# Performance work log

Hardware: AMD Instinct MI355X
Metric: run time of the kernel (lower is better)

The kernel has to match this reference:

```python
import jax, jax.numpy as jnp
import numpy as np

DIM = 256
HEADS = 8
DIM_HEAD = 32
HIDDEN = HEADS * DIM_HEAD  # 256
SCALE = DIM_HEAD ** -0.5


def setup_inputs() -> dict:
    key = jax.random.key(0)
    k1, k2, k3, k4 = jax.random.split(key, 4)
    x = jax.random.normal(k1, (1, DIM, 16, 16, 16), dtype=jnp.float32)
    # 1x1x1 Conv3d weights are plain channel-mixing matrices
    w_qkv = jax.random.normal(k2, (3 * HIDDEN, DIM), dtype=jnp.float32) * (DIM ** -0.5)
    w_out = jax.random.normal(k3, (DIM, HIDDEN), dtype=jnp.float32) * (HIDDEN ** -0.5)
    b_out = jax.random.normal(k4, (DIM,), dtype=jnp.float32) * 0.01
    return {"x": x, "w_qkv": w_qkv, "w_out": w_out, "b_out": b_out}


def reference(x, w_qkv, w_out, b_out):
    b, c, X, Y, Z = x.shape
    n = X * Y * Z
    xf = x.reshape(b, c, n)                                   # b c n
    qkv = jnp.einsum('oc,bcn->bon', w_qkv, xf)                # b 3H n
    q, k, v = jnp.split(qkv, 3, axis=1)                       # each b (h c) n
    def heads(t):
        return t.reshape(b, HEADS, DIM_HEAD, n)               # b h c n
    q, k, v = heads(q) * SCALE, heads(k), heads(v)
    sim = jnp.einsum('bhci,bhcj->bhij', q, k)                 # b h n n
    attn = jax.nn.softmax(sim, axis=-1)
    out = jnp.einsum('bhij,bhcj->bhci', attn, v)              # b h c n
    out = out.reshape(b, HIDDEN, n)                           # b (h c) n
    out = jnp.einsum('oc,bcn->bon', w_out, out) + b_out[None, :, None]
    return out.reshape(b, DIM, X, Y, Z)
```

## Files before the change

kernel.cpp:

```cpp
#include <hip/hip_runtime.h>
#include <hip/hip_bf16.h>
#include <cstdint>


typedef __bf16 bf16x8 __attribute__((ext_vector_type(8)));
typedef float f32x4 __attribute__((ext_vector_type(4)));
typedef float f32x16 __attribute__((ext_vector_type(16)));
typedef unsigned int u32;
typedef unsigned short u16;
typedef u32 u32x4v __attribute__((ext_vector_type(4)));
typedef u32 u32x2v __attribute__((ext_vector_type(2)));

#define MFMA16(a, b, c) __builtin_amdgcn_mfma_f32_16x16x32_bf16(a, b, c, 0, 0, 0)
#define MFMA32(a, b, c) __builtin_amdgcn_mfma_f32_32x32x16_bf16(a, b, c, 0, 0, 0)

#if __has_builtin(__builtin_amdgcn_exp2f)
#define EXP2(x) __builtin_amdgcn_exp2f(x)
#else
#define EXP2(x) exp2f(x)
#endif

__device__ __forceinline__ u16 f2bf(float f) {
  __bf16 b = (__bf16)f;
  return __builtin_bit_cast(u16, b);
}
__device__ __forceinline__ u32 pk2(float a, float b) {
  return (u32)f2bf(a) | ((u32)f2bf(b) << 16);
}
__device__ __forceinline__ bf16x8 ldfrag(const u16* p) {
  return __builtin_bit_cast(bf16x8, *(const u32x4v*)p);
}
__device__ __forceinline__ void gload_lds16(const void* g, void* l) {
  __builtin_amdgcn_global_load_lds((const __attribute__((address_space(1))) u32*)g,
                                   (__attribute__((address_space(3))) u32*)l, 16, 0, 0);
}
__device__ __forceinline__ void plswap(u32& a, u32& b) {
  asm("v_permlane32_swap_b32 %0, %1" : "+v"(a), "+v"(b));
}
__device__ __forceinline__ f32x16 zero16() {
  f32x16 z;
#pragma unroll
  for (int i = 0; i < 16; ++i) z[i] = 0.0f;
  return z;
}

#if __has_builtin(__builtin_amdgcn_fdot2_f32_bf16)
typedef __bf16 bf16x2 __attribute__((ext_vector_type(2)));
__device__ __forceinline__ float dot2one(u32 pk, float acc) {
  const u32 one2 = 0x3F803F80u;
  return __builtin_amdgcn_fdot2_f32_bf16(__builtin_bit_cast(bf16x2, pk),
                                         __builtin_bit_cast(bf16x2, one2), acc, false);
}
#define LSUM4(LSUM, PK0, PK1, PK2, PK3) \
  LSUM = dot2one(PK0, LSUM);            \
  LSUM = dot2one(PK1, LSUM);            \
  LSUM = dot2one(PK2, LSUM);            \
  LSUM = dot2one(PK3, LSUM);
#define LSUM_F32(LSUM, ...)
#else
#define LSUM4(LSUM, PK0, PK1, PK2, PK3)
#define LSUM_F32(LSUM, P0, P1, P2, P3, P4, P5, P6, P7) \
  LSUM += ((P0 + P1) + (P2 + P3)) + ((P4 + P5) + (P6 + P7));
#endif

__global__ __launch_bounds__(256) void prep(const float* __restrict__ x,
                                            const float* __restrict__ wq,
                                            const float* __restrict__ wo,
                                            u16* __restrict__ xT, u16* __restrict__ wqb,
                                            u16* __restrict__ wob) {
  const int b = blockIdx.x;
  const int t = threadIdx.x;
  if (b < 256) {
    __shared__ u16 tile[64][72];
    const int n0 = (b & 63) * 64, c0 = (b >> 6) * 64;
#pragma unroll
    for (int r = 0; r < 4; ++r) {
      int c = r * 16 + (t >> 4);
      int n4 = (t & 15) << 2;
      float4 v = *(const float4*)(x + (size_t)(c0 + c) * 4096 + n0 + n4);
      tile[n4 + 0][c] = f2bf(v.x);
      tile[n4 + 1][c] = f2bf(v.y);
      tile[n4 + 2][c] = f2bf(v.z);
      tile[n4 + 3][c] = f2bf(v.w);
    }
    __syncthreads();
#pragma unroll
    for (int r2 = 0; r2 < 2; ++r2) {
      int n = r2 * 32 + (t >> 3);
      int c8 = (t & 7) << 3;
      u32x4v o;
#pragma unroll
      for (int j = 0; j < 4; ++j)
        o[j] = (u32)tile[n][c8 + 2 * j] | ((u32)tile[n][c8 + 2 * j + 1] << 16);
      *(u32x4v*)(xT + (size_t)(n0 + n) * 256 + c0 + c8) = o;
    }
  } else if (b < 304) {
    int base = (b - 256) * 4096;
#pragma unroll
    for (int r = 0; r < 4; ++r) {
      int i = base + r * 1024 + t * 4;
      float4 v = *(const float4*)(wq + i);
      float sc = (i < 65536) ? 0.2550349f : 1.0f;
      u32x2v pkd;
      pkd.x = pk2(v.x * sc, v.y * sc);
      pkd.y = pk2(v.z * sc, v.w * sc);
      *(u32x2v*)(wqb + i) = pkd;
    }
  } else {
    int base = (b - 304) * 4096;
#pragma unroll
    for (int r = 0; r < 4; ++r) {
      int i = base + r * 1024 + t * 4;
      float4 v = *(const float4*)(wo + i);
      u32x2v pkd;
      pkd.x = pk2(v.x, v.y);
      pkd.y = pk2(v.z, v.w);
      *(u32x2v*)(wob + i) = pkd;
    }
  }
}

__global__ __launch_bounds__(256) void qkv_gemm(const u16* __restrict__ xT,
                                                const u16* __restrict__ wqb,
                                                u16* __restrict__ qT, u16* __restrict__ kT,
                                                u16* __restrict__ vv) {
  __shared__ __align__(16) u16 Al[64 * 64];
  __shared__ __align__(16) u16 Bl[64 * 64];
  const int t = threadIdx.x;
  const int lane = t & 63, w = t >> 6;
  const int wm = w & 1, wn = w >> 1;
  const int o0 = blockIdx.y * 64, n0 = blockIdx.x * 64;
  const int lr = lane & 15, lg = lane >> 4;
  const int srow = lane >> 3, sslot = lane & 7;
  f32x4 acc[2][2];
#pragma unroll
  for (int i = 0; i < 2; ++i)
#pragma unroll
    for (int j = 0; j < 2; ++j)
#pragma unroll
      for (int r = 0; r < 4; ++r) acc[i][j][r] = 0.0f;

  for (int kc = 0; kc < 256; kc += 64) {
#pragma unroll
    for (int rnd = 0; rnd < 2; ++rnd) {
      int row = rnd * 32 + w * 8 + srow;
      gload_lds16(wqb + (size_t)(o0 + row) * 256 + kc + ((sslot ^ (row & 7)) << 3),
                  (void*)(Al + rnd * 2048 + w * 512));
      gload_lds16(xT + (size_t)(n0 + row) * 256 + kc + ((sslot ^ (row & 7)) << 3),
                  (void*)(Bl + rnd * 2048 + w * 512));
    }
    __syncthreads();
#pragma unroll
    for (int kk = 0; kk < 2; ++kk) {
      bf16x8 af[2], bf_[2];
#pragma unroll
      for (int mi = 0; mi < 2; ++mi) {
        int row = wm * 32 + mi * 16 + lr;
        af[mi] = ldfrag(&Al[row * 64 + ((kk * 32 + lg * 8) ^ ((row & 7) << 3))]);
      }
#pragma unroll
      for (int ni = 0; ni < 2; ++ni) {
        int row = wn * 32 + ni * 16 + lr;
        bf_[ni] = ldfrag(&Bl[row * 64 + ((kk * 32 + lg * 8) ^ ((row & 7) << 3))]);
      }
#pragma unroll
      for (int mi = 0; mi < 2; ++mi)
#pragma unroll
        for (int ni = 0; ni < 2; ++ni) acc[mi][ni] = MFMA16(af[mi], bf_[ni], acc[mi][ni]);
    }
    __syncthreads();
  }
#pragma unroll
  for (int mi = 0; mi < 2; ++mi) {
#pragma unroll
    for (int ni = 0; ni < 2; ++ni) {
      int obase = o0 + wm * 32 + mi * 16 + lg * 4;
      int n = n0 + wn * 32 + ni * 16 + lr;
      int part = obase >> 8;
      int oin = obase & 255;
      int h = oin >> 5, c0 = oin & 31;
      if (part == 0) {
        u32x2v pv;
        pv.x = pk2(acc[mi][ni][0], acc[mi][ni][1]);
        pv.y = pk2(acc[mi][ni][2], acc[mi][ni][3]);
        *(u32x2v*)(qT + ((size_t)h * 4096 + n) * 32 + c0) = pv;
      } else if (part == 1) {
        u32x2v pv;
        pv.x = pk2(acc[mi][ni][0], acc[mi][ni][1]);
        pv.y = pk2(acc[mi][ni][2], acc[mi][ni][3]);
        *(u32x2v*)(kT + ((size_t)h * 4096 + n) * 32 + c0) = pv;
      } else {
#pragma unroll
        for (int r = 0; r < 4; ++r)
          vv[((size_t)h * 32 + c0 + r) * 4096 + n] = f2bf(acc[mi][ni][r]);
      }
    }
  }
}


#define QK2(ST, QA, QB, K0, K1)         \
  do {                                  \
    ST = zero16();                      \
    __builtin_amdgcn_s_setprio(1);      \
    ST = MFMA32(K0, QA, ST);            \
    ST = MFMA32(K1, QB, ST);            \
    __builtin_amdgcn_s_setprio(0);      \
  } while (0)

#define SM_PV(ST, LO, OACC, LSUM, VF)                                           \
  do {                                                                          \
    float p0_ = EXP2(ST[LO + 0]), p1_ = EXP2(ST[LO + 1]);                       \
    float p2_ = EXP2(ST[LO + 2]), p3_ = EXP2(ST[LO + 3]);                       \
    float p4_ = EXP2(ST[LO + 4]), p5_ = EXP2(ST[LO + 5]);                       \
    float p6_ = EXP2(ST[LO + 6]), p7_ = EXP2(ST[LO + 7]);                       \
    u32 k0_ = pk2(p0_, p1_), k1_ = pk2(p2_, p3_);                               \
    u32 k2_ = pk2(p4_, p5_), k3_ = pk2(p6_, p7_);                               \
    LSUM4(LSUM, k0_, k1_, k2_, k3_)                                             \
    LSUM_F32(LSUM, p0_, p1_, p2_, p3_, p4_, p5_, p6_, p7_)                      \
    u32 ax_ = k0_, bx_ = k2_;                                                   \
    plswap(ax_, bx_);                                                           \
    u32 ay_ = k1_, by_ = k3_;                                                   \
    plswap(ay_, by_);                                                           \
    u32x4v f_;                                                                  \
    f_.x = ax_; f_.y = ay_; f_.z = bx_; f_.w = by_;                             \
    __builtin_amdgcn_s_setprio(1);                                              \
    OACC = MFMA32(VF, __builtin_bit_cast(bf16x8, f_), OACC);                    \
    __builtin_amdgcn_s_setprio(0);                                              \
  } while (0)

__global__ __launch_bounds__(512, 4) void attn_fused(const u16* __restrict__ qT,
                                                     const u16* __restrict__ kT,
                                                     const u16* __restrict__ vv,
                                                     u16* __restrict__ aout) {
  __shared__ float pbuf[8 * 32 * 66];
  __shared__ float lbuf[8 * 64];
  const int tid = threadIdx.x;
  const int lane = tid & 63, s = tid >> 6;
  const int h = blockIdx.x & 7, qb = blockIdx.x >> 3;
  const int l31 = lane & 31, lh = lane >> 5;
  const u16* qTh = qT + (size_t)h * (4096 * 32);
  const u16* kTh = kT + (size_t)h * (4096 * 32);
  const u16* vh = vv + (size_t)h * (32 * 4096);

  const int i0 = qb * 64 + l31;
  bf16x8 qf00 = ldfrag(qTh + (size_t)i0 * 32 + lh * 8);
  bf16x8 qf01 = ldfrag(qTh + (size_t)i0 * 32 + 16 + lh * 8);
  bf16x8 qf10 = ldfrag(qTh + (size_t)(i0 + 32) * 32 + lh * 8);
  bf16x8 qf11 = ldfrag(qTh + (size_t)(i0 + 32) * 32 + 16 + lh * 8);

  f32x16 oacc0 = zero16(), oacc1 = zero16();
  float lsum0 = 0.0f, lsum1 = 0.0f;
  const int kvbase = s * 512;

  const u16* kp0 = kTh + (size_t)(kvbase + l31) * 32 + lh * 8;
  const u16* vp0 = vh + (size_t)l31 * 4096 + kvbase + lh * 8;

  bf16x8 kb0[3], kb1[3], vb0[3], vb1[3];
#pragma unroll
  for (int j = 0; j < 3; ++j) {
    kb0[j] = ldfrag(kp0 + j * 1024);
    kb1[j] = ldfrag(kp0 + j * 1024 + 16);
    vb0[j] = ldfrag(vp0 + j * 32);
    vb1[j] = ldfrag(vp0 + j * 32 + 16);
  }

#pragma unroll
  for (int tt = 0; tt < 16; ++tt) {
    const int sl = tt % 3;
    f32x16 sT;
    QK2(sT, qf00, qf01, kb0[sl], kb1[sl]);
    SM_PV(sT, 0, oacc0, lsum0, vb0[sl]);
    SM_PV(sT, 8, oacc0, lsum0, vb1[sl]);
    QK2(sT, qf10, qf11, kb0[sl], kb1[sl]);
    kb0[sl] = ldfrag(kp0 + (tt + 3) * 1024);
    kb1[sl] = ldfrag(kp0 + (tt + 3) * 1024 + 16);
    SM_PV(sT, 0, oacc1, lsum1, vb0[sl]);
    vb0[sl] = ldfrag(vp0 + (tt + 3) * 32);
    SM_PV(sT, 8, oacc1, lsum1, vb1[sl]);
    vb1[sl] = ldfrag(vp0 + (tt + 3) * 32 + 16);
  }

  float ls0 = lsum0 + __shfl_xor(lsum0, 32, 64);
  float ls1 = lsum1 + __shfl_xor(lsum1, 32, 64);
#pragma unroll
  for (int r = 0; r < 16; ++r) {
    int c = (r & 3) + 8 * (r >> 2) + 4 * lh;
    pbuf[(s * 32 + c) * 66 + l31] = oacc0[r];
    pbuf[(s * 32 + c) * 66 + 32 + l31] = oacc1[r];
  }
  lbuf[s * 64 + l31] = ls0;
  lbuf[s * 64 + 32 + l31] = ls1;
  __syncthreads();

  {
    int i = tid >> 3, c0 = (tid & 7) << 2;
    float lt = 0.0f;
#pragma unroll
    for (int ss = 0; ss < 8; ++ss) lt += lbuf[ss * 64 + i];
    float inv = 1.0f / lt;
    float a[4];
#pragma unroll
    for (int cc = 0; cc < 4; ++cc) a[cc] = 0.0f;
#pragma unroll
    for (int ss = 0; ss < 8; ++ss)
#pragma unroll
      for (int cc = 0; cc < 4; ++cc) a[cc] += pbuf[(ss * 32 + c0 + cc) * 66 + i];
    u32x2v ov;
    ov.x = pk2(a[0] * inv, a[1] * inv);
    ov.y = pk2(a[2] * inv, a[3] * inv);
    *(u32x2v*)(aout + (size_t)(qb * 64 + i) * 256 + h * 32 + c0) = ov;
  }
}

__global__ __launch_bounds__(256) void out_proj(const u16* __restrict__ wob,
                                                const float* __restrict__ bo,
                                                const u16* __restrict__ aout,
                                                float* __restrict__ out) {
  __shared__ __align__(16) u16 Al[64 * 64];
  __shared__ __align__(16) u16 Bl[64 * 64];
  const int t = threadIdx.x;
  const int lane = t & 63, w = t >> 6;
  const int n0 = blockIdx.x * 64, d0 = blockIdx.y * 64;
  const int lr = lane & 15, lg = lane >> 4;
  const int srow = lane >> 3, sslot = lane & 7;
  f32x4 acc[4];
#pragma unroll
  for (int ni = 0; ni < 4; ++ni)
#pragma unroll
    for (int r = 0; r < 4; ++r) acc[ni][r] = 0.0f;

  for (int kc = 0; kc < 256; kc += 64) {
#pragma unroll
    for (int rnd = 0; rnd < 2; ++rnd) {
      int row = rnd * 32 + w * 8 + srow;
      gload_lds16(wob + (size_t)(d0 + row) * 256 + kc + ((sslot ^ (row & 7)) << 3),
                  (void*)(Al + rnd * 2048 + w * 512));
      gload_lds16(aout + (size_t)(n0 + row) * 256 + kc + ((sslot ^ (row & 7)) << 3),
                  (void*)(Bl + rnd * 2048 + w * 512));
    }
    __syncthreads();
#pragma unroll
    for (int kk = 0; kk < 2; ++kk) {
      int arow = w * 16 + lr;
      bf16x8 af = ldfrag(&Al[arow * 64 + ((kk * 32 + lg * 8) ^ ((arow & 7) << 3))]);
#pragma unroll
      for (int ni = 0; ni < 4; ++ni) {
        int brow = ni * 16 + lr;
        bf16x8 bfr = ldfrag(&Bl[brow * 64 + ((kk * 32 + lg * 8) ^ ((brow & 7) << 3))]);
        acc[ni] = MFMA16(af, bfr, acc[ni]);
      }
    }
    __syncthreads();
  }
#pragma unroll
  for (int ni = 0; ni < 4; ++ni) {
    int n = n0 + ni * 16 + lr;
#pragma unroll
    for (int r = 0; r < 4; ++r) {
      int d = d0 + w * 16 + lg * 4 + r;
      out[(size_t)d * 4096 + n] = acc[ni][r] + bo[d];
    }
  }
}

extern "C" void kernel_launch(void* const* d_in, const int* in_sizes, int n_in,
                              void* d_out, int out_size, void* d_ws, size_t ws_size,
                              hipStream_t stream) {
  (void)in_sizes; (void)n_in; (void)out_size; (void)ws_size;
  const float* x = (const float*)d_in[0];
  const float* wqkv = (const float*)d_in[1];
  const float* wout = (const float*)d_in[2];
  const float* bout = (const float*)d_in[3];
  float* out = (float*)d_out;
  u16* qT = (u16*)d_ws;
  u16* kT = qT + 8 * 4096 * 32;
  u16* vv = kT + 8 * 4096 * 32;
  u16* aout = vv + 8 * 32 * 4096;
  u16* xT = aout + 4096 * 256;
  u16* wqb = xT + 4096 * 256;
  u16* wob = wqb + 768 * 256;

  prep<<<320, 256, 0, stream>>>(x, wqkv, wout, xT, wqb, wob);
  qkv_gemm<<<dim3(64, 12), 256, 0, stream>>>(xT, wqb, qT, kT, vv);
  attn_fused<<<512, 512, 0, stream>>>(qT, kT, vv, aout);
  out_proj<<<dim3(64, 4), 256, 0, stream>>>(wob, bout, aout, out);
}
```

Measured before the change: 57.34 us.

## Software-pipeline QK for next tile against softmax/PV of current tile

Restructures the attention inner loop so the QK^T MFMAs for tile t+1 are issued while the exp/pack/PV work for tile t proceeds, using two score accumulators and double-buffered V fragments. Prefetch depth drops from three buffers to two. The aim is to let the MFMA and VALU exp work overlap instead of serializing QK then softmax per tile. In exchange it holds two 16-wide score registers live at once, which adds register pressure under launch bounds of 512 threads and 4 blocks.

```diff
diff --git a/kernel.cpp b/kernel.cpp
--- a/kernel.cpp
+++ b/kernel.cpp
@@ -229,6 +229,20 @@
     __builtin_amdgcn_s_setprio(0);                                              \
   } while (0)
 
+#define STAGE(TT, VF0, VF1)                                   \
+  do {                                                        \
+    SM_PV(sTa, 0, oacc0, lsum0, VF0);                         \
+    SM_PV(sTa, 8, oacc0, lsum0, VF1);                         \
+    QK2(sTa, qf00, qf01, kfn0, kfn1);                         \
+    SM_PV(sTb, 0, oacc1, lsum1, VF0);                         \
+    SM_PV(sTb, 8, oacc1, lsum1, VF1);                         \
+    QK2(sTb, qf10, qf11, kfn0, kfn1);                         \
+    kfn0 = ldfrag(kp0 + (TT + 2) * 1024);                     \
+    kfn1 = ldfrag(kp0 + (TT + 2) * 1024 + 16);                \
+    VF0 = ldfrag(vp0 + (TT + 2) * 32);                        \
+    VF1 = ldfrag(vp0 + (TT + 2) * 32 + 16);                   \
+  } while (0)
+
 __global__ __launch_bounds__(512, 4) void attn_fused(const u16* __restrict__ qT,
                                                      const u16* __restrict__ kT,
                                                      const u16* __restrict__ vv,
@@ -256,29 +270,18 @@
   const u16* kp0 = kTh + (size_t)(kvbase + l31) * 32 + lh * 8;
   const u16* vp0 = vh + (size_t)l31 * 4096 + kvbase + lh * 8;
 
-  bf16x8 kb0[3], kb1[3], vb0[3], vb1[3];
-#pragma unroll
-  for (int j = 0; j < 3; ++j) {
-    kb0[j] = ldfrag(kp0 + j * 1024);
-    kb1[j] = ldfrag(kp0 + j * 1024 + 16);
-    vb0[j] = ldfrag(vp0 + j * 32);
-    vb1[j] = ldfrag(vp0 + j * 32 + 16);
-  }
-
-#pragma unroll
-  for (int tt = 0; tt < 16; ++tt) {
-    const int sl = tt % 3;
-    f32x16 sT;
-    QK2(sT, qf00, qf01, kb0[sl], kb1[sl]);
-    SM_PV(sT, 0, oacc0, lsum0, vb0[sl]);
-    SM_PV(sT, 8, oacc0, lsum0, vb1[sl]);
-    QK2(sT, qf10, qf11, kb0[sl], kb1[sl]);
-    kb0[sl] = ldfrag(kp0 + (tt + 3) * 1024);
-    kb1[sl] = ldfrag(kp0 + (tt + 3) * 1024 + 16);
-    SM_PV(sT, 0, oacc1, lsum1, vb0[sl]);
-    vb0[sl] = ldfrag(vp0 + (tt + 3) * 32);
-    SM_PV(sT, 8, oacc1, lsum1, vb1[sl]);
-    vb1[sl] = ldfrag(vp0 + (tt + 3) * 32 + 16);
+  bf16x8 kc0 = ldfrag(kp0), kc1 = ldfrag(kp0 + 16);
+  bf16x8 vfa0 = ldfrag(vp0), vfa1 = ldfrag(vp0 + 16);
+  bf16x8 kfn0 = ldfrag(kp0 + 1024), kfn1 = ldfrag(kp0 + 1024 + 16);
+  bf16x8 vfb0 = ldfrag(vp0 + 32), vfb1 = ldfrag(vp0 + 32 + 16);
+  f32x16 sTa, sTb;
+  QK2(sTa, qf00, qf01, kc0, kc1);
+  QK2(sTb, qf10, qf11, kc0, kc1);
+
+#pragma unroll
+  for (int tt = 0; tt < 16; tt += 2) {
+    STAGE(tt, vfa0, vfa1);
+    STAGE(tt + 1, vfb0, vfb1);
   }
 
   float ls0 = lsum0 + __shfl_xor(lsum0, 32, 64);
```

After: 48.35 us (median of 2 runs). 15.7% less time.
